# Performance work log

Hardware: AMD Instinct MI355X
Metric: run time of the kernel (lower is better)

Reference implementation:

```python
import jax, jax.numpy as jnp
import numpy as np

D_MODEL = 1024
NUM_HEADS = 16
D_K = D_MODEL // NUM_HEADS
LN_EPS = 1e-5


def setup_inputs() -> dict:
    key = jax.random.key(0)
    ks = jax.random.split(key, 9)
    s = 1.0 / np.sqrt(D_MODEL)
    x = jax.random.normal(ks[0], (4, 2048, D_MODEL), dtype=jnp.float32)
    Wq = jax.random.uniform(ks[1], (D_MODEL, D_MODEL), minval=-s, maxval=s, dtype=jnp.float32)
    bq = jax.random.uniform(ks[2], (D_MODEL,), minval=-s, maxval=s, dtype=jnp.float32)
    Wk = jax.random.uniform(ks[3], (D_MODEL, D_MODEL), minval=-s, maxval=s, dtype=jnp.float32)
    bk = jax.random.uniform(ks[4], (D_MODEL,), minval=-s, maxval=s, dtype=jnp.float32)
    Wv = jax.random.uniform(ks[5], (D_MODEL, D_MODEL), minval=-s, maxval=s, dtype=jnp.float32)
    bv = jax.random.uniform(ks[6], (D_MODEL,), minval=-s, maxval=s, dtype=jnp.float32)
    Wo = jax.random.uniform(ks[7], (D_MODEL, D_MODEL), minval=-s, maxval=s, dtype=jnp.float32)
    bo = jax.random.uniform(ks[8], (D_MODEL,), minval=-s, maxval=s, dtype=jnp.float32)
    gamma = jnp.ones((D_MODEL,), dtype=jnp.float32)
    beta = jnp.zeros((D_MODEL,), dtype=jnp.float32)
    return {"x": x, "Wq": Wq, "bq": bq, "Wk": Wk, "bk": bk, "Wv": Wv, "bv": bv,
            "Wo": Wo, "bo": bo, "gamma": gamma, "beta": beta}


def reference(x, Wq, bq, Wk, bk, Wv, bv, Wo, bo, gamma, beta):
    B, S, D = x.shape
    H, dk = NUM_HEADS, D_K
    # torch Linear: y = x @ W^T + b; split heads -> (B, H, S, dk)
    def proj(W, b):
        return (jnp.einsum('bsd,ed->bse', x, W) + b).reshape(B, S, H, dk).transpose(0, 2, 1, 3)
    Q = proj(Wq, bq)
    K = proj(Wk, bk)
    V = proj(Wv, bv)
    scores = jnp.einsum('bhqd,bhkd->bhqk', Q, K) / jnp.sqrt(jnp.float32(dk))
    attn = jax.nn.softmax(scores, axis=-1)  # dropout is identity in eval mode
    ctx = jnp.einsum('bhqk,bhkd->bhqd', attn, V)
    ctx = ctx.transpose(0, 2, 1, 3).reshape(B, S, D)
    out = jnp.einsum('bsd,ed->bse', ctx, Wo) + bo
    y = out + x
    mu = jnp.mean(y, axis=-1, keepdims=True)
    var = jnp.mean(jnp.square(y - mu), axis=-1, keepdims=True)
    return (y - mu) * jax.lax.rsqrt(var + LN_EPS) * gamma + beta
```

## Files before the change

### kernel.cpp

```cpp
#include <hip/hip_runtime.h>


#define SEQ 2048
#define DMODEL 1024
#define NH 16
#define DK 64
#define NROWS 8192

typedef unsigned short u16;
typedef unsigned int u32;
typedef __bf16 bf16;
typedef bf16 bf16x8 __attribute__((ext_vector_type(8)));
typedef float f32x4 __attribute__((ext_vector_type(4)));
typedef float f32x16 __attribute__((ext_vector_type(16)));
typedef unsigned u32x2 __attribute__((ext_vector_type(2)));

__device__ inline u16 bfbits(float f) { return __builtin_bit_cast(u16, (bf16)f); }
__device__ inline u32 packbf2(float a, float b) {
    return (u32)bfbits(a) | ((u32)bfbits(b) << 16);
}

__device__ inline float sexp2(float s) {
    return __builtin_bit_cast(float, (u32)(int)fmaf(s, 8388608.0f, 1064986823.0f));
}

__device__ inline void gload16(const u16* g, u16* l) {
    __builtin_amdgcn_global_load_lds(
        (const __attribute__((address_space(1))) u32*)g,
        (__attribute__((address_space(3))) u32*)l, 16, 0, 0);
}

__device__ inline void plswap(u32& a, u32& b) {
#if __has_builtin(__builtin_amdgcn_permlane32_swap)
    u32x2 r = __builtin_amdgcn_permlane32_swap(a, b, false, false);
    a = r[0]; b = r[1];
#else
    u32 xa = __shfl_xor(a, 32), xb = __shfl_xor(b, 32);
    int hi = (threadIdx.x & 63) >> 5;
    u32 na = hi ? xb : a;
    u32 nb = hi ? b : xa;
    a = na; b = nb;
#endif
}

__global__ __launch_bounds__(256) void cvt_f32_bf16(const float* __restrict__ in,
                                                    u16* __restrict__ out, int n) {
    int i = (blockIdx.x * 256 + threadIdx.x) * 4;
    if (i >= n) return;
    float4 v = *(const float4*)(in + i);
    ushort4 o;
    o.x = bfbits(v.x); o.y = bfbits(v.y); o.z = bfbits(v.z); o.w = bfbits(v.w);
    *(ushort4*)(out + i) = o;
}

__global__ __launch_bounds__(256) void cvt4_w(const float* __restrict__ w0,
                                              const float* __restrict__ w1,
                                              const float* __restrict__ w2,
                                              const float* __restrict__ w3,
                                              u16* __restrict__ o0, u16* __restrict__ o1,
                                              u16* __restrict__ o2, u16* __restrict__ o3) {
    const float* in;
    u16* out;
    switch (blockIdx.y) {
        case 0: in = w0; out = o0; break;
        case 1: in = w1; out = o1; break;
        case 2: in = w2; out = o2; break;
        default: in = w3; out = o3; break;
    }
    int i = (blockIdx.x * 256 + threadIdx.x) * 4;
    float4 v = *(const float4*)(in + i);
    ushort4 o;
    o.x = bfbits(v.x); o.y = bfbits(v.y); o.z = bfbits(v.z); o.w = bfbits(v.w);
    *(ushort4*)(out + i) = o;
}

template <int EPI>
__global__ __launch_bounds__(256) void gemm_bt(
    const u16* __restrict__ A, const u16* __restrict__ Bm,
    const float* __restrict__ bias0, const float* __restrict__ bias1,
    const float* __restrict__ bias2,
    u16* __restrict__ Qo, u16* __restrict__ Ko, u16* __restrict__ Vo,
    const float* __restrict__ xres, float* __restrict__ yout) {
    __shared__ __align__(16) u16 smem[16384];
    u16* As = smem;
    u16* Bs = smem + 8192;

    const int tid  = threadIdx.x;
    const int lane = tid & 63;
    const int w    = tid >> 6;
    const int wr   = (w >> 1) * 64;
    const int wc   = (w & 1) * 64;
    const int l16  = lane & 15;
    const int lq   = lane >> 4;
    const int m0   = blockIdx.x * 128;
    const int n0   = blockIdx.y * 128;

    f32x4 acc[4][4];
#pragma unroll
    for (int m = 0; m < 4; m++)
#pragma unroll
        for (int n = 0; n < 4; n++) {
            f32x4 z = {0.f, 0.f, 0.f, 0.f};
            acc[m][n] = z;
        }

    const int l8r = lane >> 3;
    const int sch = (lane & 7) ^ l8r;
    const u16* a_g = A  + (size_t)(m0 + w * 32 + l8r) * 1024 + sch * 8;
    const u16* b_g = Bm + (size_t)(n0 + w * 32 + l8r) * 1024 + sch * 8;

    for (int k0 = 0; k0 < 1024; k0 += 64) {
        __syncthreads();
#pragma unroll
        for (int i = 0; i < 4; i++) {
            gload16(a_g + (size_t)i * 8192 + k0, As + (w * 32 + i * 8) * 64);
            gload16(b_g + (size_t)i * 8192 + k0, Bs + (w * 32 + i * 8) * 64);
        }
        __syncthreads();

#pragma unroll
        for (int kk = 0; kk < 2; kk++) {
            bf16x8 af[4], bfr[4];
#pragma unroll
            for (int m = 0; m < 4; m++)
                af[m] = *(const bf16x8*)&As[(wr + m * 16 + l16) * 64 +
                                            (((kk << 2) | lq) ^ (l16 & 7)) * 8];
#pragma unroll
            for (int n = 0; n < 4; n++)
                bfr[n] = *(const bf16x8*)&Bs[(wc + n * 16 + l16) * 64 +
                                             (((kk << 2) | lq) ^ (l16 & 7)) * 8];
            __builtin_amdgcn_s_setprio(1);
#pragma unroll
            for (int m = 0; m < 4; m++)
#pragma unroll
                for (int n = 0; n < 4; n++)
                    acc[m][n] = __builtin_amdgcn_mfma_f32_16x16x32_bf16(
                        af[m], bfr[n], acc[m][n], 0, 0, 0);
            __builtin_amdgcn_s_setprio(0);
        }
    }

    if (EPI == 0 && n0 >= 2048) {
        const int e0 = n0 - 2048;
        __syncthreads();
#pragma unroll
        for (int m = 0; m < 4; m++)
#pragma unroll
            for (int n = 0; n < 4; n++) {
                const int col = wc + n * 16 + l16;
                const int row = wr + lq * 4 + m * 16;
                const float bias = bias2[e0 + col];
                ushort4 pk;
                pk.x = bfbits(acc[m][n][0] + bias);
                pk.y = bfbits(acc[m][n][1] + bias);
                pk.z = bfbits(acc[m][n][2] + bias);
                pk.w = bfbits(acc[m][n][3] + bias);
                *(ushort4*)&smem[col * 128 + (row ^ ((col & 7) << 3))] = pk;
            }
        __syncthreads();
        const int b = m0 >> 11;
        const int sbase = m0 & 2047;
#pragma unroll
        for (int i = 0; i < 8; i++) {
            const int c = tid + 256 * i;
            const int col = c >> 4;
            const int s0 = (c & 15) * 8;
            uint4 val = *(const uint4*)&smem[col * 128 + (s0 ^ ((col & 7) << 3))];
            const int eg = e0 + col;
            const int bh = b * NH + (eg >> 6);
            *(uint4*)&Vo[((size_t)bh * DK + (eg & 63)) * SEQ + sbase + s0] = val;
        }
        return;
    }

    const int rbase = m0 + wr + lq * 4;
    const int cbase = n0 + wc + l16;
#pragma unroll
    for (int m = 0; m < 4; m++)
#pragma unroll
        for (int n = 0; n < 4; n++) {
            const int col = cbase + n * 16;
#pragma unroll
            for (int r = 0; r < 4; r++) {
                const int row = rbase + m * 16 + r;
                float v = acc[m][n][r];
                if (EPI == 0) {
                    const int which = col >> 10;
                    const int e = col & 1023;
                    v += (which == 0) ? bias0[e] : bias1[e];
                    if (which == 0) v *= 0.18033688011112042f;
                    const int h = e >> 6, d = e & 63;
                    const int b = row >> 11, s = row & 2047;
                    const int bh = b * NH + h;
                    if (which == 0)
                        Qo[((size_t)bh * SEQ + s) * DK + d] = bfbits(v);
                    else
                        Ko[((size_t)bh * SEQ + s) * DK + d] = bfbits(v);
                } else {
                    v += bias0[col] + xres[(size_t)row * DMODEL + col];
                    yout[(size_t)row * DMODEL + col] = v;
                }
            }
        }
}

__global__ __launch_bounds__(512) void attn(const u16* __restrict__ Qb,
                                            const u16* __restrict__ Kb,
                                            const u16* __restrict__ Vtb,
                                            u16* __restrict__ ctx) {
    __shared__ __align__(16) u16 smem[16384];

    const int tid  = threadIdx.x;
    const int lane = tid & 63;
    const int w    = tid >> 6;
    const int q    = lane & 31;
    const int hi   = lane >> 5;
    const int bh   = blockIdx.x;
    const int q0   = blockIdx.y * 256 + w * 32;

    const u16* qp = Qb + ((size_t)bh * SEQ + q0 + q) * DK + hi * 8;
    bf16x8 qf0 = *(const bf16x8*)(qp);
    bf16x8 qf1 = *(const bf16x8*)(qp + 16);
    bf16x8 qf2 = *(const bf16x8*)(qp + 32);
    bf16x8 qf3 = *(const bf16x8*)(qp + 48);

    const int l8r = lane >> 3;
    const int sch = (lane & 7) ^ l8r;
    const u16* kg = Kb  + ((size_t)bh * SEQ + w * 8 + l8r) * 64 + sch * 8;
    const u16* vg = Vtb + ((size_t)bh * DK  + w * 8 + l8r) * SEQ + sch * 8;
    u16* kl = smem + w * 512;
    u16* vl = smem + 8192 + w * 512;

    f32x16 oacc0, oacc1;
#pragma unroll
    for (int r = 0; r < 16; r++) { oacc0[r] = 0.f; oacc1[r] = 0.f; }
    f32x16 fzero;
#pragma unroll
    for (int r = 0; r < 16; r++) fzero[r] = 0.f;
    float l_ = 0.f;

    gload16(kg, kl);
    gload16(vg, vl);
    __syncthreads();

    for (int t = 0; t < SEQ / 64; t++) {
        if (t < SEQ / 64 - 1) {
            gload16(kg + (size_t)(t + 1) * 4096, kl + ((t + 1) & 1) * 4096);
            gload16(vg + (size_t)(t + 1) * 64,  vl + ((t + 1) & 1) * 4096);
        }
        const u16* Kl = smem + (t & 1) * 4096;
        const u16* Vl = smem + 8192 + (t & 1) * 4096;

        f32x16 sacc0, sacc1;
        {
            bf16x8 k00 = *(const bf16x8*)&Kl[(q)      * 64 + ((0 | hi) ^ (q & 7)) * 8];
            bf16x8 k01 = *(const bf16x8*)&Kl[(q)      * 64 + ((2 | hi) ^ (q & 7)) * 8];
            bf16x8 k02 = *(const bf16x8*)&Kl[(q)      * 64 + ((4 | hi) ^ (q & 7)) * 8];
            bf16x8 k03 = *(const bf16x8*)&Kl[(q)      * 64 + ((6 | hi) ^ (q & 7)) * 8];
            bf16x8 k10 = *(const bf16x8*)&Kl[(q + 32) * 64 + ((0 | hi) ^ (q & 7)) * 8];
            bf16x8 k11 = *(const bf16x8*)&Kl[(q + 32) * 64 + ((2 | hi) ^ (q & 7)) * 8];
            bf16x8 k12 = *(const bf16x8*)&Kl[(q + 32) * 64 + ((4 | hi) ^ (q & 7)) * 8];
            bf16x8 k13 = *(const bf16x8*)&Kl[(q + 32) * 64 + ((6 | hi) ^ (q & 7)) * 8];
            __builtin_amdgcn_s_setprio(1);
            sacc0 = __builtin_amdgcn_mfma_f32_32x32x16_bf16(k00, qf0, fzero, 0, 0, 0);
            sacc1 = __builtin_amdgcn_mfma_f32_32x32x16_bf16(k10, qf0, fzero, 0, 0, 0);
            sacc0 = __builtin_amdgcn_mfma_f32_32x32x16_bf16(k01, qf1, sacc0, 0, 0, 0);
            sacc1 = __builtin_amdgcn_mfma_f32_32x32x16_bf16(k11, qf1, sacc1, 0, 0, 0);
            sacc0 = __builtin_amdgcn_mfma_f32_32x32x16_bf16(k02, qf2, sacc0, 0, 0, 0);
            sacc1 = __builtin_amdgcn_mfma_f32_32x32x16_bf16(k12, qf2, sacc1, 0, 0, 0);
            sacc0 = __builtin_amdgcn_mfma_f32_32x32x16_bf16(k03, qf3, sacc0, 0, 0, 0);
            sacc1 = __builtin_amdgcn_mfma_f32_32x32x16_bf16(k13, qf3, sacc1, 0, 0, 0);
            __builtin_amdgcn_s_setprio(0);
        }

#pragma unroll
        for (int r = 0; r < 16; r++) sacc0[r] = sexp2(sacc0[r]);
#pragma unroll
        for (int r = 0; r < 16; r++) sacc1[r] = sexp2(sacc1[r]);
        {
            float s0 = ((sacc0[0] + sacc0[1]) + (sacc0[2] + sacc0[3])) +
                       ((sacc0[4] + sacc0[5]) + (sacc0[6] + sacc0[7]));
            float s1 = ((sacc0[8] + sacc0[9]) + (sacc0[10] + sacc0[11])) +
                       ((sacc0[12] + sacc0[13]) + (sacc0[14] + sacc0[15]));
            float s2 = ((sacc1[0] + sacc1[1]) + (sacc1[2] + sacc1[3])) +
                       ((sacc1[4] + sacc1[5]) + (sacc1[6] + sacc1[7]));
            float s3 = ((sacc1[8] + sacc1[9]) + (sacc1[10] + sacc1[11])) +
                       ((sacc1[12] + sacc1[13]) + (sacc1[14] + sacc1[15]));
            l_ += (s0 + s1) + (s2 + s3);
        }

        u32 wa[8], wb[8];
#pragma unroll
        for (int i = 0; i < 8; i++) wa[i] = packbf2(sacc0[2 * i], sacc0[2 * i + 1]);
#pragma unroll
        for (int i = 0; i < 8; i++) wb[i] = packbf2(sacc1[2 * i], sacc1[2 * i + 1]);
        plswap(wa[0], wa[2]); plswap(wa[1], wa[3]);
        plswap(wa[4], wa[6]); plswap(wa[5], wa[7]);
        plswap(wb[0], wb[2]); plswap(wb[1], wb[3]);
        plswap(wb[4], wb[6]); plswap(wb[5], wb[7]);
        union { u32 u[4]; bf16x8 v; } pf0, pf1, pf2, pf3;
        pf0.u[0] = wa[0]; pf0.u[1] = wa[1]; pf0.u[2] = wa[2]; pf0.u[3] = wa[3];
        pf1.u[0] = wa[4]; pf1.u[1] = wa[5]; pf1.u[2] = wa[6]; pf1.u[3] = wa[7];
        pf2.u[0] = wb[0]; pf2.u[1] = wb[1]; pf2.u[2] = wb[2]; pf2.u[3] = wb[3];
        pf3.u[0] = wb[4]; pf3.u[1] = wb[5]; pf3.u[2] = wb[6]; pf3.u[3] = wb[7];

        {
            bf16x8 v00 = *(const bf16x8*)&Vl[(q)      * 64 + ((0 | hi) ^ (q & 7)) * 8];
            bf16x8 v01 = *(const bf16x8*)&Vl[(q)      * 64 + ((2 | hi) ^ (q & 7)) * 8];
            bf16x8 v02 = *(const bf16x8*)&Vl[(q)      * 64 + ((4 | hi) ^ (q & 7)) * 8];
            bf16x8 v03 = *(const bf16x8*)&Vl[(q)      * 64 + ((6 | hi) ^ (q & 7)) * 8];
            bf16x8 v10 = *(const bf16x8*)&Vl[(q + 32) * 64 + ((0 | hi) ^ (q & 7)) * 8];
            bf16x8 v11 = *(const bf16x8*)&Vl[(q + 32) * 64 + ((2 | hi) ^ (q & 7)) * 8];
            bf16x8 v12 = *(const bf16x8*)&Vl[(q + 32) * 64 + ((4 | hi) ^ (q & 7)) * 8];
            bf16x8 v13 = *(const bf16x8*)&Vl[(q + 32) * 64 + ((6 | hi) ^ (q & 7)) * 8];
            __builtin_amdgcn_s_setprio(1);
            oacc0 = __builtin_amdgcn_mfma_f32_32x32x16_bf16(v00, pf0.v, oacc0, 0, 0, 0);
            oacc1 = __builtin_amdgcn_mfma_f32_32x32x16_bf16(v10, pf0.v, oacc1, 0, 0, 0);
            oacc0 = __builtin_amdgcn_mfma_f32_32x32x16_bf16(v01, pf1.v, oacc0, 0, 0, 0);
            oacc1 = __builtin_amdgcn_mfma_f32_32x32x16_bf16(v11, pf1.v, oacc1, 0, 0, 0);
            oacc0 = __builtin_amdgcn_mfma_f32_32x32x16_bf16(v02, pf2.v, oacc0, 0, 0, 0);
            oacc1 = __builtin_amdgcn_mfma_f32_32x32x16_bf16(v12, pf2.v, oacc1, 0, 0, 0);
            oacc0 = __builtin_amdgcn_mfma_f32_32x32x16_bf16(v03, pf3.v, oacc0, 0, 0, 0);
            oacc1 = __builtin_amdgcn_mfma_f32_32x32x16_bf16(v13, pf3.v, oacc1, 0, 0, 0);
            __builtin_amdgcn_s_setprio(0);
        }

        __syncthreads();
    }

    const float lfull = l_ + __shfl_xor(l_, 32);
    const float invl = 1.f / lfull;
    const int wbase = w * 2048;
#pragma unroll
    for (int r = 0; r < 16; r++) {
        const int dk0 = (r & 3) + 8 * (r >> 2) + 4 * hi;
        const int dk1 = 32 + dk0;
        smem[wbase + q * 64 + (((dk0 >> 3) ^ (q & 7)) << 3) + (dk0 & 7)] = bfbits(oacc0[r] * invl);
        smem[wbase + q * 64 + (((dk1 >> 3) ^ (q & 7)) << 3) + (dk1 & 7)] = bfbits(oacc1[r] * invl);
    }
    __syncthreads();
    const int b = bh >> 4, h = bh & 15;
    const int r4 = lane >> 1;
    const int cc = (lane & 1) * 4;
#pragma unroll
    for (int c = 0; c < 4; c++) {
        const int chunk = cc + c;
        uint4 val = *(const uint4*)&smem[wbase + r4 * 64 + ((chunk ^ (r4 & 7)) << 3)];
        *(uint4*)&ctx[((size_t)(b * SEQ + q0 + r4)) * DMODEL + h * DK + chunk * 8] = val;
    }
}

__global__ __launch_bounds__(256) void ln_inplace(float* __restrict__ y,
                                                  const float* __restrict__ gamma,
                                                  const float* __restrict__ beta) {
    const int row = blockIdx.x;
    float* p = y + (size_t)row * DMODEL;
    const int tid = threadIdx.x;
    float4 v = *(const float4*)(p + tid * 4);
    float s  = v.x + v.y + v.z + v.w;
    float sq = v.x * v.x + v.y * v.y + v.z * v.z + v.w * v.w;
#pragma unroll
    for (int m = 1; m < 64; m <<= 1) {
        s  += __shfl_xor(s, m);
        sq += __shfl_xor(sq, m);
    }
    __shared__ float rs[4], rq[4];
    if ((tid & 63) == 0) { rs[tid >> 6] = s; rq[tid >> 6] = sq; }
    __syncthreads();
    s  = rs[0] + rs[1] + rs[2] + rs[3];
    sq = rq[0] + rq[1] + rq[2] + rq[3];
    const float mean = s * (1.0f / 1024.0f);
    const float var  = sq * (1.0f / 1024.0f) - mean * mean;
    const float inv  = rsqrtf(var + 1e-5f);
    const int c = tid * 4;
    float4 g4 = *(const float4*)(gamma + c);
    float4 b4 = *(const float4*)(beta + c);
    float4 o;
    o.x = (v.x - mean) * inv * g4.x + b4.x;
    o.y = (v.y - mean) * inv * g4.y + b4.y;
    o.z = (v.z - mean) * inv * g4.z + b4.z;
    o.w = (v.w - mean) * inv * g4.w + b4.w;
    *(float4*)(p + c) = o;
}

extern "C" void kernel_launch(void* const* d_in, const int* in_sizes, int n_in,
                              void* d_out, int out_size, void* d_ws, size_t ws_size,
                              hipStream_t stream) {
    const float* x     = (const float*)d_in[0];
    const float* Wq    = (const float*)d_in[1];
    const float* bq    = (const float*)d_in[2];
    const float* Wk    = (const float*)d_in[3];
    const float* bk    = (const float*)d_in[4];
    const float* Wv    = (const float*)d_in[5];
    const float* bv    = (const float*)d_in[6];
    const float* Wo    = (const float*)d_in[7];
    const float* bo    = (const float*)d_in[8];
    const float* gamma = (const float*)d_in[9];
    const float* beta  = (const float*)d_in[10];
    float* out = (float*)d_out;

    u16* x_bf    = (u16*)d_ws;
    u16* Wqkv_bf = x_bf + (size_t)NROWS * DMODEL;
    u16* Wo_bf   = Wqkv_bf + (size_t)3072 * 1024;
    u16* Q_bf    = Wo_bf + (size_t)1024 * 1024;
    u16* K_bf    = Q_bf + (size_t)64 * SEQ * DK;
    u16* Vt_bf   = K_bf + (size_t)64 * SEQ * DK;
    u16* ctx_bf  = x_bf;

    cvt_f32_bf16<<<8192, 256, 0, stream>>>(x, x_bf, NROWS * DMODEL);
    cvt4_w<<<dim3(1024, 4), 256, 0, stream>>>(Wq, Wk, Wv, Wo,
                                              Wqkv_bf, Wqkv_bf + 1048576,
                                              Wqkv_bf + 2097152, Wo_bf);

    gemm_bt<0><<<dim3(64, 24), 256, 0, stream>>>(x_bf, Wqkv_bf,
                                                 bq, bk, bv, Q_bf, K_bf, Vt_bf,
                                                 nullptr, nullptr);
    attn<<<dim3(64, 8), 512, 0, stream>>>(Q_bf, K_bf, Vt_bf, ctx_bf);
    gemm_bt<1><<<dim3(64, 8), 256, 0, stream>>>(ctx_bf, Wo_bf,
                                                bo, nullptr, nullptr,
                                                nullptr, nullptr, nullptr,
                                                x, out);
    ln_inplace<<<8192, 256, 0, stream>>>(out, gamma, beta);
}
```

Baseline: 204.6 us.

## Double-buffer GEMM tiles with async LDS loads and merge conversion kernels

The GEMM kernel now uses 512 threads and a two-stage LDS double buffer. The next-but-one k-tile is prefetched with global_load_lds and the loop waits on vmcnt, so loads overlap with MFMA work instead of sitting behind a full sync each iteration. Each wave now covers 32 rows instead of 64, which halves the accumulators per thread, and the QK epilogue hoists the bias load and index math out of the row loop. The x and weight conversion kernels are merged into a single launch. The cost is double the LDS per block, which may limit occupancy.

```diff
diff --git a/kernel.cpp b/kernel.cpp
--- a/kernel.cpp
+++ b/kernel.cpp
@@ -43,61 +43,57 @@
 #endif
 }
 
-__global__ __launch_bounds__(256) void cvt_f32_bf16(const float* __restrict__ in,
-                                                    u16* __restrict__ out, int n) {
-    int i = (blockIdx.x * 256 + threadIdx.x) * 4;
-    if (i >= n) return;
+__global__ __launch_bounds__(256) void cvt_all(
+    const float* __restrict__ x,  const float* __restrict__ w0,
+    const float* __restrict__ w1, const float* __restrict__ w2,
+    const float* __restrict__ w3,
+    u16* __restrict__ xo, u16* __restrict__ o0, u16* __restrict__ o1,
+    u16* __restrict__ o2, u16* __restrict__ o3) {
+    const int b = blockIdx.x;
+    const float* in;
+    u16* out;
+    int base;
+    if (b < 8192) {
+        in = x; out = xo; base = b << 10;
+    } else {
+        const int wsel = (b - 8192) >> 10;
+        base = ((b - 8192) & 1023) << 10;
+        switch (wsel) {
+            case 0: in = w0; out = o0; break;
+            case 1: in = w1; out = o1; break;
+            case 2: in = w2; out = o2; break;
+            default: in = w3; out = o3; break;
+        }
+    }
+    const int i = base + threadIdx.x * 4;
     float4 v = *(const float4*)(in + i);
     ushort4 o;
     o.x = bfbits(v.x); o.y = bfbits(v.y); o.z = bfbits(v.z); o.w = bfbits(v.w);
     *(ushort4*)(out + i) = o;
 }
 
-__global__ __launch_bounds__(256) void cvt4_w(const float* __restrict__ w0,
-                                              const float* __restrict__ w1,
-                                              const float* __restrict__ w2,
-                                              const float* __restrict__ w3,
-                                              u16* __restrict__ o0, u16* __restrict__ o1,
-                                              u16* __restrict__ o2, u16* __restrict__ o3) {
-    const float* in;
-    u16* out;
-    switch (blockIdx.y) {
-        case 0: in = w0; out = o0; break;
-        case 1: in = w1; out = o1; break;
-        case 2: in = w2; out = o2; break;
-        default: in = w3; out = o3; break;
-    }
-    int i = (blockIdx.x * 256 + threadIdx.x) * 4;
-    float4 v = *(const float4*)(in + i);
-    ushort4 o;
-    o.x = bfbits(v.x); o.y = bfbits(v.y); o.z = bfbits(v.z); o.w = bfbits(v.w);
-    *(ushort4*)(out + i) = o;
-}
-
 template <int EPI>
-__global__ __launch_bounds__(256) void gemm_bt(
+__global__ __launch_bounds__(512) void gemm_piped(
     const u16* __restrict__ A, const u16* __restrict__ Bm,
     const float* __restrict__ bias0, const float* __restrict__ bias1,
     const float* __restrict__ bias2,
     u16* __restrict__ Qo, u16* __restrict__ Ko, u16* __restrict__ Vo,
     const float* __restrict__ xres, float* __restrict__ yout) {
-    __shared__ __align__(16) u16 smem[16384];
-    u16* As = smem;
-    u16* Bs = smem + 8192;
+    __shared__ __align__(16) u16 smem[32768];
 
     const int tid  = threadIdx.x;
     const int lane = tid & 63;
     const int w    = tid >> 6;
-    const int wr   = (w >> 1) * 64;
+    const int wr   = (w >> 1) * 32;
     const int wc   = (w & 1) * 64;
     const int l16  = lane & 15;
     const int lq   = lane >> 4;
     const int m0   = blockIdx.x * 128;
     const int n0   = blockIdx.y * 128;
 
-    f32x4 acc[4][4];
-#pragma unroll
-    for (int m = 0; m < 4; m++)
+    f32x4 acc[2][4];
+#pragma unroll
+    for (int m = 0; m < 2; m++)
 #pragma unroll
         for (int n = 0; n < 4; n++) {
             f32x4 z = {0.f, 0.f, 0.f, 0.f};
@@ -106,45 +102,58 @@
 
     const int l8r = lane >> 3;
     const int sch = (lane & 7) ^ l8r;
-    const u16* a_g = A  + (size_t)(m0 + w * 32 + l8r) * 1024 + sch * 8;
-    const u16* b_g = Bm + (size_t)(n0 + w * 32 + l8r) * 1024 + sch * 8;
-
-    for (int k0 = 0; k0 < 1024; k0 += 64) {
-        __syncthreads();
-#pragma unroll
-        for (int i = 0; i < 4; i++) {
-            gload16(a_g + (size_t)i * 8192 + k0, As + (w * 32 + i * 8) * 64);
-            gload16(b_g + (size_t)i * 8192 + k0, Bs + (w * 32 + i * 8) * 64);
-        }
-        __syncthreads();
-
+    const u16* a_g = A  + (size_t)(m0 + w * 8 + l8r) * 1024 + sch * 8;
+    const u16* b_g = Bm + (size_t)(n0 + w * 8 + l8r) * 1024 + sch * 8;
+    u16* asd = smem + w * 512;
+    u16* bsd = smem + 16384 + w * 512;
+
+#define STAGE(kt, c) do {                                              \
+        gload16(a_g + (kt) * 64,         asd + (c) * 8192);            \
+        gload16(a_g + 65536 + (kt) * 64, asd + (c) * 8192 + 4096);     \
+        gload16(b_g + (kt) * 64,         bsd + (c) * 8192);            \
+        gload16(b_g + 65536 + (kt) * 64, bsd + (c) * 8192 + 4096);     \
+    } while (0)
+
+    STAGE(0, 0);
+    STAGE(1, 1);
+
+    for (int kt = 0; kt < 16; kt++) {
+        const int cur = kt & 1;
+        if (kt < 15) asm volatile("s_waitcnt vmcnt(4)" ::: "memory");
+        else         asm volatile("s_waitcnt vmcnt(0)" ::: "memory");
+        __builtin_amdgcn_s_barrier();
+
+        const u16* Asl = smem + cur * 8192;
+        const u16* Bsl = smem + 16384 + cur * 8192;
 #pragma unroll
         for (int kk = 0; kk < 2; kk++) {
-            bf16x8 af[4], bfr[4];
-#pragma unroll
-            for (int m = 0; m < 4; m++)
-                af[m] = *(const bf16x8*)&As[(wr + m * 16 + l16) * 64 +
-                                            (((kk << 2) | lq) ^ (l16 & 7)) * 8];
+            bf16x8 af[2], bfr[4];
+#pragma unroll
+            for (int m = 0; m < 2; m++)
+                af[m] = *(const bf16x8*)&Asl[(wr + m * 16 + l16) * 64 +
+                                             (((kk << 2) | lq) ^ (l16 & 7)) * 8];
 #pragma unroll
             for (int n = 0; n < 4; n++)
-                bfr[n] = *(const bf16x8*)&Bs[(wc + n * 16 + l16) * 64 +
-                                             (((kk << 2) | lq) ^ (l16 & 7)) * 8];
+                bfr[n] = *(const bf16x8*)&Bsl[(wc + n * 16 + l16) * 64 +
+                                              (((kk << 2) | lq) ^ (l16 & 7)) * 8];
             __builtin_amdgcn_s_setprio(1);
 #pragma unroll
-            for (int m = 0; m < 4; m++)
+            for (int m = 0; m < 2; m++)
 #pragma unroll
                 for (int n = 0; n < 4; n++)
                     acc[m][n] = __builtin_amdgcn_mfma_f32_16x16x32_bf16(
                         af[m], bfr[n], acc[m][n], 0, 0, 0);
             __builtin_amdgcn_s_setprio(0);
         }
-    }
+        __builtin_amdgcn_s_barrier();
+        if (kt < 14) STAGE(kt + 2, cur);
+    }
+#undef STAGE
 
     if (EPI == 0 && n0 >= 2048) {
         const int e0 = n0 - 2048;
-        __syncthreads();
-#pragma unroll
-        for (int m = 0; m < 4; m++)
+#pragma unroll
+        for (int m = 0; m < 2; m++)
 #pragma unroll
             for (int n = 0; n < 4; n++) {
                 const int col = wc + n * 16 + l16;
@@ -161,8 +170,8 @@
         const int b = m0 >> 11;
         const int sbase = m0 & 2047;
 #pragma unroll
-        for (int i = 0; i < 8; i++) {
-            const int c = tid + 256 * i;
+        for (int i = 0; i < 4; i++) {
+            const int c = tid + 512 * i;
             const int col = c >> 4;
             const int s0 = (c & 15) * 8;
             uint4 val = *(const uint4*)&smem[col * 128 + (s0 ^ ((col & 7) << 3))];
@@ -174,30 +183,33 @@
     }
 
     const int rbase = m0 + wr + lq * 4;
-    const int cbase = n0 + wc + l16;
-#pragma unroll
-    for (int m = 0; m < 4; m++)
+#pragma unroll
+    for (int m = 0; m < 2; m++)
 #pragma unroll
         for (int n = 0; n < 4; n++) {
-            const int col = cbase + n * 16;
-#pragma unroll
-            for (int r = 0; r < 4; r++) {
-                const int row = rbase + m * 16 + r;
-                float v = acc[m][n][r];
-                if (EPI == 0) {
-                    const int which = col >> 10;
-                    const int e = col & 1023;
-                    v += (which == 0) ? bias0[e] : bias1[e];
+            if (EPI == 0) {
+                const int which = n0 >> 10;
+                const int e = (n0 & 1023) + wc + n * 16 + l16;
+                const float bias = (which == 0) ? bias0[e] : bias1[e];
+                const int h = e >> 6, d = e & 63;
+#pragma unroll
+                for (int r = 0; r < 4; r++) {
+                    const int row = rbase + m * 16 + r;
+                    float v = acc[m][n][r] + bias;
                     if (which == 0) v *= 0.18033688011112042f;
-                    const int h = e >> 6, d = e & 63;
                     const int b = row >> 11, s = row & 2047;
                     const int bh = b * NH + h;
                     if (which == 0)
                         Qo[((size_t)bh * SEQ + s) * DK + d] = bfbits(v);
                     else
                         Ko[((size_t)bh * SEQ + s) * DK + d] = bfbits(v);
-                } else {
-                    v += bias0[col] + xres[(size_t)row * DMODEL + col];
+                }
+            } else {
+                const int col = n0 + wc + n * 16 + l16;
+#pragma unroll
+                for (int r = 0; r < 4; r++) {
+                    const int row = rbase + m * 16 + r;
+                    float v = acc[m][n][r] + bias0[col] + xres[(size_t)row * DMODEL + col];
                     yout[(size_t)row * DMODEL + col] = v;
                 }
             }
@@ -407,18 +419,17 @@
     u16* Vt_bf   = K_bf + (size_t)64 * SEQ * DK;
     u16* ctx_bf  = x_bf;
 
-    cvt_f32_bf16<<<8192, 256, 0, stream>>>(x, x_bf, NROWS * DMODEL);
-    cvt4_w<<<dim3(1024, 4), 256, 0, stream>>>(Wq, Wk, Wv, Wo,
-                                              Wqkv_bf, Wqkv_bf + 1048576,
-                                              Wqkv_bf + 2097152, Wo_bf);
-
-    gemm_bt<0><<<dim3(64, 24), 256, 0, stream>>>(x_bf, Wqkv_bf,
-                                                 bq, bk, bv, Q_bf, K_bf, Vt_bf,
-                                                 nullptr, nullptr);
+    cvt_all<<<12288, 256, 0, stream>>>(x, Wq, Wk, Wv, Wo,
+                                       x_bf, Wqkv_bf, Wqkv_bf + 1048576,
+                                       Wqkv_bf + 2097152, Wo_bf);
+
+    gemm_piped<0><<<dim3(64, 24), 512, 0, stream>>>(x_bf, Wqkv_bf,
+                                                    bq, bk, bv, Q_bf, K_bf, Vt_bf,
+                                                    nullptr, nullptr);
     attn<<<dim3(64, 8), 512, 0, stream>>>(Q_bf, K_bf, Vt_bf, ctx_bf);
-    gemm_bt<1><<<dim3(64, 8), 256, 0, stream>>>(ctx_bf, Wo_bf,
-                                                bo, nullptr, nullptr,
-                                                nullptr, nullptr, nullptr,
-                                                x, out);
+    gemm_piped<1><<<dim3(64, 8), 512, 0, stream>>>(ctx_bf, Wo_bf,
+                                                   bo, nullptr, nullptr,
+                                                   nullptr, nullptr, nullptr,
+                                                   x, out);
     ln_inplace<<<8192, 256, 0, stream>>>(out, gamma, beta);
 }
```

After: 194.1 us. 5.1% less time.
